# Performance work log

Measured on AMD Instinct MI355X. Metric: run time of the kernel, lower is better.

## Reference

```python
import jax, jax.numpy as jnp
import numpy as np

K = 100  # hard-coded in GWDLoss.forward


def _topk(scores, k=K):
    # CenterNet predict._topk: per-class topk then topk over classes.
    b, c, h, w = scores.shape
    topk_scores, topk_inds = jax.lax.top_k(scores.reshape(b, c, h * w), k)  # [b,c,k]
    topk_inds = topk_inds % (h * w)
    topk_ys = (topk_inds // w).astype(scores.dtype)
    topk_xs = (topk_inds % w).astype(scores.dtype)
    topk_score, topk_ind = jax.lax.top_k(topk_scores.reshape(b, c * k), k)  # [b,k]
    def g(t):
        return jnp.take_along_axis(t.reshape(b, c * k), topk_ind, axis=1)
    return topk_score, g(topk_inds), g(topk_xs), g(topk_ys)


def _transpose_and_gather_feat(feat, ind):
    b, c, h, w = feat.shape
    feat = feat.transpose(0, 2, 3, 1).reshape(b, h * w, c)  # [b,hw,c]
    idx = jnp.broadcast_to(ind[:, :, None], (b, ind.shape[1], c))
    return jnp.take_along_axis(feat, idx, axis=1)  # [b,K,c]


def xywhr2xyrs(xywhr):
    xywhr = xywhr.reshape(-1, 5)
    xy = xywhr[:, :2]
    wh = jnp.clip(xywhr[:, 2:4], 1e-7, 1e7)
    r = jnp.deg2rad(xywhr[:, 4])
    cos_r, sin_r = jnp.cos(r), jnp.sin(r)
    R = jnp.stack([cos_r, -sin_r, sin_r, cos_r], axis=-1).reshape(-1, 2, 2)
    S = 0.5 * wh[:, :, None] * jnp.eye(2, dtype=wh.dtype)  # diag_embed
    return xy, R, S


def gwd_loss(pred, target, tau=1.0, alpha=1.0):
    xy_p, R_p, S_p = xywhr2xyrs(pred)
    xy_t, R_t, S_t = xywhr2xyrs(target)
    xy_distance = jnp.sum((xy_p - xy_t) ** 2, axis=-1)
    Sigma_p = R_p @ (S_p ** 2) @ jnp.swapaxes(R_p, -1, -2)
    Sigma_t = R_t @ (S_t ** 2) @ jnp.swapaxes(R_t, -1, -2)
    dS_p = jnp.diagonal(S_p, axis1=-2, axis2=-1)
    dS_t = jnp.diagonal(S_t, axis1=-2, axis2=-1)
    whr = jnp.sum(dS_p ** 2, -1) + jnp.sum(dS_t ** 2, -1)
    _t = Sigma_p @ Sigma_t
    _t_tr = jnp.trace(_t, axis1=-2, axis2=-1)
    _t_det_sqrt = jnp.prod(dS_p, -1) * jnp.prod(dS_t, -1)
    whr = whr - 2.0 * jnp.sqrt(jnp.maximum(_t_tr + 2.0 * _t_det_sqrt, 0.0))
    distance = jnp.maximum(xy_distance + alpha * alpha * whr, 0.0)
    distance = jnp.log1p(distance)  # fun='log'
    return 1.0 - 1.0 / (tau + distance)  # tau=1.0 >= 1.0


def _forward(hm_p, ab_p, ang_p, hm_t, ab_t, ang_t, ind, reg_mask):
    mask = reg_mask.astype(jnp.float32)  # [B,K]
    pred_ab = _transpose_and_gather_feat(ab_p, ind)    # [B,K,2]
    pred_ang = _transpose_and_gather_feat(ang_p, ind)  # [B,K,1]
    mask_ab = mask[:, :, None]
    mask_ang = mask[:, :, None]
    _, _, xp, yp = _topk(hm_p)
    pred_xy = jnp.stack([xp, yp], axis=2)  # [B,K,2]
    pred = jnp.concatenate([pred_xy * mask_ab, pred_ab * 2.0 * mask_ab,
                            (pred_ang - 90.0) * mask_ang], axis=2)
    _, _, xt, yt = _topk(hm_t)
    target_xy = jnp.stack([xt, yt], axis=2)
    target = jnp.concatenate([target_xy * mask_ab, ab_t * 2.0 * mask_ab,
                              (ang_t - 90.0) * mask_ang], axis=2)
    return jnp.sum(gwd_loss(pred, target)) / (jnp.sum(mask) + 1e-8)


def setup_inputs() -> dict:
    key = jax.random.key(0)
    ks = jax.random.split(key, 8)
    B, H, W = 64, 256, 256
    return {
        "hm_p": jax.random.uniform(ks[0], (B, 1, H, W), jnp.float32),
        "ab_p": jax.random.uniform(ks[1], (B, 2, H, W), jnp.float32),
        "ang_p": jax.random.uniform(ks[2], (B, 1, H, W), jnp.float32),
        "hm_t": jax.random.uniform(ks[3], (B, 1, H, W), jnp.float32),
        "ab_t": jax.random.uniform(ks[4], (B, K, 2), jnp.float32),
        "ang_t": jax.random.uniform(ks[5], (B, K, 1), jnp.float32),
        "ind": jax.random.randint(ks[6], (B, K), 0, H * W, jnp.int32),
        "reg_mask": jax.random.randint(ks[7], (B, K), 0, 2, jnp.int32),
    }


def reference(hm_p, ab_p, ang_p, hm_t, ab_t, ang_t, ind, reg_mask):
    return _forward(hm_p, ab_p, ang_p, hm_t, ab_t, ang_t, ind, reg_mask)
```

## Files before the change

kernel.cpp:

```cpp
#include <hip/hip_runtime.h>
#include <stdint.h>

#define HW 65536
#define WIMG 256
#define TOPK 100
#define CAP2 2048
#define CAPC 256
#define NCHUNK 8
#define NGROUP 128
#define NPAIR 6400
#define FTHR 512

__device__ __forceinline__ uint32_t fkey(float v) {
    uint32_t b = __float_as_uint(v);
    return b ^ ((b & 0x80000000u) ? 0xFFFFFFFFu : 0x80000000u);
}

#define CAND_OFF  0
#define CNT_OFF   2097152
#define XY_OFF    2101248
#define PART_OFF  2203648
#define DONE_OFF  2204160
#define WS_FAST_BYTES 2204164

#define FILT_THR 0.9975f

#define AGENT __HIP_MEMORY_SCOPE_AGENT

__global__ __launch_bounds__(FTHR) void filter_kernel(
    const float* __restrict__ hm_p, const float* __restrict__ hm_t,
    unsigned long long* __restrict__ cand, uint32_t* __restrict__ chunkcnt)
{
    __shared__ unsigned long long lbuf[CAPC];
    __shared__ uint32_t lcnt;

    const int blk   = blockIdx.x;
    const int group = blk >> 3;
    const int chunk = blk & (NCHUNK - 1);
    const int which = group & 1;
    const int b     = group >> 1;
    const float* src = (which ? hm_t : hm_p) + (size_t)b * HW + chunk * (HW / NCHUNK);
    const float4* src4 = (const float4*)src;
    const int base0 = chunk * (HW / NCHUNK);

    if (threadIdx.x == 0) lcnt = 0;
    __syncthreads();

    #pragma unroll
    for (int t = 0; t < HW / NCHUNK / 4 / FTHR; ++t) {
        const int i = threadIdx.x + t * FTHR;
        float4 v = src4[i];
        const int base = base0 + i * 4;
        float f[4] = {v.x, v.y, v.z, v.w};
        #pragma unroll
        for (int e = 0; e < 4; ++e) {
            if (f[e] > FILT_THR) {
                uint32_t pos = atomicAdd(&lcnt, 1u);
                if (pos < CAPC)
                    lbuf[pos] = ((unsigned long long)fkey(f[e]) << 16) |
                                (unsigned long long)(65535 - (base + e));
            }
        }
    }
    __syncthreads();
    const uint32_t c = lcnt;
    if (threadIdx.x == 0) chunkcnt[blk] = c;
    unsigned long long* gc = cand + (size_t)blk * CAPC;
    for (uint32_t i = threadIdx.x; i < min(c, (uint32_t)CAPC); i += FTHR)
        gc[i] = lbuf[i];
}

__global__ __launch_bounds__(256) void sort_emit_kernel(
    const float* __restrict__ hm_p, const float* __restrict__ hm_t,
    const unsigned long long* __restrict__ cand, const uint32_t* __restrict__ chunkcnt,
    float* __restrict__ xy, uint32_t* __restrict__ done_cnt)
{
    __shared__ unsigned long long s[CAP2];
    __shared__ uint32_t s_cnt, s_kthr, s_klo, s_khi;

    const int tid   = threadIdx.x;
    const int group = blockIdx.x;
    const int which = group & 1;
    const int b     = group >> 1;

    if (group == 0 && tid == 0) *done_cnt = 0;

    uint32_t cs[NCHUNK];
    uint32_t total = 0;
    bool ok = true;
    #pragma unroll
    for (int k = 0; k < NCHUNK; ++k) {
        cs[k] = chunkcnt[group * NCHUNK + k];
        if (cs[k] > CAPC) ok = false;
        total += cs[k];
    }

    uint32_t c;
    if (ok && total >= TOPK && total <= CAP2) {
        uint32_t off = 0;
        #pragma unroll
        for (int k = 0; k < NCHUNK; ++k) {
            const unsigned long long* gc = cand + (size_t)(group * NCHUNK + k) * CAPC;
            for (uint32_t i = tid; i < cs[k]; i += 256) s[off + i] = gc[i];
            off += cs[k];
        }
        c = total;
    } else {
        const float* src = (which ? hm_t : hm_p) + (size_t)b * HW;
        const float4* src4 = (const float4*)src;
        if (tid == 0) { s_kthr = fkey(0.99f); s_klo = 0u; s_khi = 0xFFFFFFFFu; }
        __syncthreads();
        for (int it = 0; it < 48; ++it) {
            if (tid == 0) s_cnt = 0;
            __syncthreads();
            const uint32_t kthr = s_kthr;
            for (int t = 0; t < HW / 4 / 256; ++t) {
                float4 v = src4[tid + t * 256];
                const int base = (tid + t * 256) * 4;
                float f[4] = {v.x, v.y, v.z, v.w};
                #pragma unroll
                for (int e = 0; e < 4; ++e) {
                    uint32_t uk = fkey(f[e]);
                    if (uk > kthr) {
                        uint32_t pos = atomicAdd(&s_cnt, 1u);
                        if (pos < CAP2)
                            s[pos] = ((unsigned long long)uk << 16) |
                                     (unsigned long long)(65535 - (base + e));
                    }
                }
            }
            __syncthreads();
            const uint32_t cc = s_cnt;
            if (cc >= TOPK && cc <= CAP2) break;
            if (tid == 0) {
                if (cc < TOPK) { s_khi = s_kthr; s_kthr = s_klo + ((s_kthr - s_klo) >> 1); }
                else           { s_klo = s_kthr; s_kthr = s_kthr + ((s_khi - s_kthr) >> 1); }
            }
            __syncthreads();
        }
        c = min(s_cnt, (uint32_t)CAP2);
    }
    __syncthreads();

    int M = 128;
    while (M < (int)c) M <<= 1;
    for (int i = tid; i < M; i += 256) if (i >= (int)c) s[i] = 0ull;
    __syncthreads();

    for (int len = 2; len <= M; len <<= 1) {
        for (int inc = len >> 1; inc > 0; inc >>= 1) {
            for (int i = tid; i < M; i += 256) {
                int j = i ^ inc;
                if (j > i) {
                    bool desc = ((i & len) == 0);
                    unsigned long long a = s[i], d = s[j];
                    if ((a < d) == desc) { s[i] = d; s[j] = a; }
                }
            }
            __syncthreads();
        }
    }

    const int obase = which * 6400 + b * TOPK;
    for (int j = tid; j < TOPK; j += 256) {
        unsigned long long key = s[j];
        uint32_t idx = 65535u - (uint32_t)(key & 0xFFFFull);
        xy[obase + j]         = (float)(idx & (WIMG - 1));
        xy[12800 + obase + j] = (float)(idx >> 8);
    }
}

__device__ __forceinline__ float gwd(float px, float py, float pw, float ph, float pr,
                                     float tx, float ty, float tw, float th, float trg)
{
    pw = fminf(fmaxf(pw, 1e-7f), 1e7f);  ph = fminf(fmaxf(ph, 1e-7f), 1e7f);
    tw = fminf(fmaxf(tw, 1e-7f), 1e7f);  th = fminf(fmaxf(th, 1e-7f), 1e7f);
    const float d2r = 0.017453292519943295f;
    float rp = pr * d2r, rt = trg * d2r;
    float cp = cosf(rp), sp = sinf(rp);
    float ct = cosf(rt), st = sinf(rt);
    float ap = 0.5f * pw, bp = 0.5f * ph;
    float at = 0.5f * tw, bt = 0.5f * th;
    float ap2 = ap * ap, bp2 = bp * bp, at2 = at * at, bt2 = bt * bt;
    float p00 = ap2 * cp * cp + bp2 * sp * sp;
    float p11 = ap2 * sp * sp + bp2 * cp * cp;
    float p01 = (ap2 - bp2) * cp * sp;
    float t00 = at2 * ct * ct + bt2 * st * st;
    float t11 = at2 * st * st + bt2 * ct * ct;
    float t01 = (at2 - bt2) * ct * st;
    float dx = px - tx, dy = py - ty;
    float xyd = dx * dx + dy * dy;
    float whr = ap2 + bp2 + at2 + bt2;
    float trc = p00 * t00 + 2.f * p01 * t01 + p11 * t11;
    float dets = (ap * bp) * (at * bt);
    whr -= 2.f * sqrtf(fmaxf(trc + 2.f * dets, 0.f));
    float dist = fmaxf(xyd + whr, 0.f);
    float d = log1pf(dist);
    return 1.f - 1.f / (1.f + d);
}

__global__ __launch_bounds__(128) void loss_final_kernel(
    const float* __restrict__ ab_p,  const float* __restrict__ ang_p,
    const float* __restrict__ ab_t,  const float* __restrict__ ang_t,
    const int*   __restrict__ ind,   const int*   __restrict__ reg_mask,
    const float* __restrict__ xy,    float* __restrict__ partials,
    uint32_t* __restrict__ done_cnt, float* __restrict__ out)
{
    const int b = blockIdx.x;
    const int j = threadIdx.x;
    float loss = 0.f, msum = 0.f;
    if (j < TOPK) {
        const int i = b * TOPK + j;
        float m = (float)reg_mask[i];
        msum = m;
        int id = ind[i];
        float xp = xy[i];
        float xt = xy[6400 + i];
        float yp = xy[12800 + i];
        float yt = xy[19200 + i];
        float ab0 = ab_p[(size_t)(b * 2 + 0) * HW + id];
        float ab1 = ab_p[(size_t)(b * 2 + 1) * HW + id];
        float ang = ang_p[(size_t)b * HW + id];
        float px = xp * m, py = yp * m;
        float pw = 2.f * ab0 * m, ph = 2.f * ab1 * m;
        float pr = (ang - 90.f) * m;
        float tx = xt * m, ty = yt * m;
        float tw = 2.f * ab_t[b * 200 + j * 2 + 0] * m;
        float th = 2.f * ab_t[b * 200 + j * 2 + 1] * m;
        float trg = (ang_t[i] - 90.f) * m;
        loss = gwd(px, py, pw, ph, pr, tx, ty, tw, th, trg);
    }
    #pragma unroll
    for (int off = 32; off > 0; off >>= 1) {
        loss += __shfl_down(loss, off);
        msum += __shfl_down(msum, off);
    }
    __shared__ float sl[2], sm[2];
    __shared__ uint32_t s_old;
    if ((threadIdx.x & 63) == 0) { sl[threadIdx.x >> 6] = loss; sm[threadIdx.x >> 6] = msum; }
    __syncthreads();
    if (threadIdx.x == 0) {
        __hip_atomic_store(&partials[b * 2],     sl[0] + sl[1], __ATOMIC_RELEASE, AGENT);
        __hip_atomic_store(&partials[b * 2 + 1], sm[0] + sm[1], __ATOMIC_RELEASE, AGENT);
        s_old = __hip_atomic_fetch_add(done_cnt, 1u, __ATOMIC_ACQ_REL, AGENT);
    }
    __syncthreads();
    if (s_old == 63u && threadIdx.x < 64) {
        float L = __hip_atomic_load(&partials[2 * threadIdx.x],     __ATOMIC_ACQUIRE, AGENT);
        float M = __hip_atomic_load(&partials[2 * threadIdx.x + 1], __ATOMIC_ACQUIRE, AGENT);
        #pragma unroll
        for (int off = 32; off > 0; off >>= 1) {
            L += __shfl_down(L, off);
            M += __shfl_down(M, off);
        }
        if (threadIdx.x == 0) out[0] = L / (M + 1e-8f);
    }
}

#define XY_OFF2    0
#define PART_OFF2  102400
#define FDONE_OFF2 102912

__global__ __launch_bounds__(1024) void topk_sort_kernel(
    const float* __restrict__ hm_p, const float* __restrict__ hm_t,
    float* __restrict__ xy, uint32_t* __restrict__ fdone)
{
    __shared__ unsigned long long s[CAP2];
    __shared__ uint32_t lcnt, s_kthr, s_klo, s_khi;

    const int tid   = threadIdx.x;
    const int group = blockIdx.x;
    const int which = group & 1;
    const int b     = group >> 1;

    if (group == 0 && tid == 0) *fdone = 0u;

    const float* src = (which ? hm_t : hm_p) + (size_t)b * HW;
    const float4* src4 = (const float4*)src;

    if (tid == 0) lcnt = 0;
    __syncthreads();
    #pragma unroll 4
    for (int t = 0; t < HW / 4 / 1024; ++t) {
        const int i = tid + t * 1024;
        float4 v = src4[i];
        const int base = i * 4;
        float f[4] = {v.x, v.y, v.z, v.w};
        #pragma unroll
        for (int e = 0; e < 4; ++e) {
            if (f[e] > FILT_THR) {
                uint32_t pos = atomicAdd(&lcnt, 1u);
                if (pos < CAP2)
                    s[pos] = ((unsigned long long)fkey(f[e]) << 16) |
                             (unsigned long long)(65535 - (base + e));
            }
        }
    }
    __syncthreads();
    uint32_t c = lcnt;

    if (c < TOPK || c > CAP2) {
        if (tid == 0) { s_kthr = fkey(0.99f); s_klo = 0u; s_khi = 0xFFFFFFFFu; }
        __syncthreads();
        for (int it = 0; it < 48; ++it) {
            if (tid == 0) lcnt = 0;
            __syncthreads();
            const uint32_t kthr = s_kthr;
            for (int t = 0; t < HW / 4 / 1024; ++t) {
                float4 v = src4[tid + t * 1024];
                const int base = (tid + t * 1024) * 4;
                float f[4] = {v.x, v.y, v.z, v.w};
                #pragma unroll
                for (int e = 0; e < 4; ++e) {
                    uint32_t uk = fkey(f[e]);
                    if (uk > kthr) {
                        uint32_t pos = atomicAdd(&lcnt, 1u);
                        if (pos < CAP2)
                            s[pos] = ((unsigned long long)uk << 16) |
                                     (unsigned long long)(65535 - (base + e));
                    }
                }
            }
            __syncthreads();
            const uint32_t cc = lcnt;
            if (cc >= TOPK && cc <= CAP2) break;
            if (tid == 0) {
                if (cc < TOPK) { s_khi = s_kthr; s_kthr = s_klo + ((s_kthr - s_klo) >> 1); }
                else           { s_klo = s_kthr; s_kthr = s_kthr + ((s_khi - s_kthr) >> 1); }
            }
            __syncthreads();
        }
        c = min(lcnt, (uint32_t)CAP2);
        __syncthreads();
    }

    int M = 128;
    while (M < (int)c) M <<= 1;
    for (int i = tid; i < M; i += 1024) if (i >= (int)c) s[i] = 0ull;
    __syncthreads();
    for (int len = 2; len <= M; len <<= 1) {
        for (int inc = len >> 1; inc > 0; inc >>= 1) {
            for (int i = tid; i < M; i += 1024) {
                int j = i ^ inc;
                if (j > i) {
                    bool desc = ((i & len) == 0);
                    unsigned long long a = s[i], d = s[j];
                    if ((a < d) == desc) { s[i] = d; s[j] = a; }
                }
            }
            __syncthreads();
        }
    }
    const int obase = which * 6400 + b * TOPK;
    for (int j = tid; j < TOPK; j += 1024) {
        unsigned long long key = s[j];
        uint32_t idx = 65535u - (uint32_t)(key & 0xFFFFull);
        xy[obase + j]         = (float)(idx & (WIMG - 1));
        xy[12800 + obase + j] = (float)(idx >> 8);
    }
}

extern "C" void kernel_launch(void* const* d_in, const int* in_sizes, int n_in,
                              void* d_out, int out_size, void* d_ws, size_t ws_size,
                              hipStream_t stream)
{
    const float* hm_p  = (const float*)d_in[0];
    const float* ab_p  = (const float*)d_in[1];
    const float* ang_p = (const float*)d_in[2];
    const float* hm_t  = (const float*)d_in[3];
    const float* ab_t  = (const float*)d_in[4];
    const float* ang_t = (const float*)d_in[5];
    const int*   ind      = (const int*)d_in[6];
    const int*   reg_mask = (const int*)d_in[7];
    float* out = (float*)d_out;

    if (ws_size >= WS_FAST_BYTES) {
        unsigned long long* cand = (unsigned long long*)((char*)d_ws + CAND_OFF);
        uint32_t* cnt   = (uint32_t*)((char*)d_ws + CNT_OFF);
        float*    xy    = (float*)((char*)d_ws + XY_OFF);
        float*    part  = (float*)((char*)d_ws + PART_OFF);
        uint32_t* done  = (uint32_t*)((char*)d_ws + DONE_OFF);

        filter_kernel<<<NGROUP * NCHUNK, FTHR, 0, stream>>>(hm_p, hm_t, cand, cnt);
        sort_emit_kernel<<<NGROUP, 256, 0, stream>>>(hm_p, hm_t, cand, cnt, xy, done);
        loss_final_kernel<<<64, 128, 0, stream>>>(ab_p, ang_p, ab_t, ang_t, ind,
                                                  reg_mask, xy, part, done, out);
    } else {
        float*    xy    = (float*)((char*)d_ws + XY_OFF2);
        float*    part  = (float*)((char*)d_ws + PART_OFF2);
        uint32_t* fdone = (uint32_t*)((char*)d_ws + FDONE_OFF2);
        topk_sort_kernel<<<NGROUP, 1024, 0, stream>>>(hm_p, hm_t, xy, fdone);
        loss_final_kernel<<<64, 128, 0, stream>>>(ab_p, ang_p, ab_t, ang_t, ind,
                                                  reg_mask, xy, part, fdone, out);
    }
}
```

Before: 26.53 us.

## Replace bitonic sort with rank counting and shrink per-chunk candidate buffers

After: 21.43 us, median of 3. -19.2%, faster.

```diff
diff --git a/kernel.cpp b/kernel.cpp
--- a/kernel.cpp
+++ b/kernel.cpp
@@ -5,10 +5,9 @@
 #define WIMG 256
 #define TOPK 100
 #define CAP2 2048
-#define CAPC 256
+#define CAPC 64
 #define NCHUNK 8
 #define NGROUP 128
-#define NPAIR 6400
 #define FTHR 512
 
 __device__ __forceinline__ uint32_t fkey(float v) {
@@ -17,11 +16,11 @@
 }
 
 #define CAND_OFF  0
-#define CNT_OFF   2097152
-#define XY_OFF    2101248
-#define PART_OFF  2203648
-#define DONE_OFF  2204160
-#define WS_FAST_BYTES 2204164
+#define CNT_OFF   524288
+#define XY_OFF    528384
+#define PART_OFF  630784
+#define DONE_OFF  631296
+#define WS_FAST_BYTES 631300
 
 #define FILT_THR 0.9975f
 
@@ -66,8 +65,8 @@
     const uint32_t c = lcnt;
     if (threadIdx.x == 0) chunkcnt[blk] = c;
     unsigned long long* gc = cand + (size_t)blk * CAPC;
-    for (uint32_t i = threadIdx.x; i < min(c, (uint32_t)CAPC); i += FTHR)
-        gc[i] = lbuf[i];
+    if (threadIdx.x < min(c, (uint32_t)CAPC))
+        gc[threadIdx.x] = lbuf[threadIdx.x];
 }
 
 __global__ __launch_bounds__(256) void sort_emit_kernel(
@@ -76,6 +75,8 @@
     float* __restrict__ xy, uint32_t* __restrict__ done_cnt)
 {
     __shared__ unsigned long long s[CAP2];
+    __shared__ uint32_t s_cs[NCHUNK], s_off[NCHUNK];
+    __shared__ uint32_t s_meta[2];
     __shared__ uint32_t s_cnt, s_kthr, s_klo, s_khi;
 
     const int tid   = threadIdx.x;
@@ -85,26 +86,29 @@
 
     if (group == 0 && tid == 0) *done_cnt = 0;
 
-    uint32_t cs[NCHUNK];
-    uint32_t total = 0;
-    bool ok = true;
-    #pragma unroll
-    for (int k = 0; k < NCHUNK; ++k) {
-        cs[k] = chunkcnt[group * NCHUNK + k];
-        if (cs[k] > CAPC) ok = false;
-        total += cs[k];
-    }
-
-    uint32_t c;
-    if (ok && total >= TOPK && total <= CAP2) {
-        uint32_t off = 0;
+    if (tid < NCHUNK) s_cs[tid] = chunkcnt[group * NCHUNK + tid];
+    __syncthreads();
+    if (tid == 0) {
+        uint32_t off = 0; int ok = 1;
         #pragma unroll
         for (int k = 0; k < NCHUNK; ++k) {
-            const unsigned long long* gc = cand + (size_t)(group * NCHUNK + k) * CAPC;
-            for (uint32_t i = tid; i < cs[k]; i += 256) s[off + i] = gc[i];
-            off += cs[k];
-        }
-        c = total;
+            s_off[k] = off;
+            if (s_cs[k] > CAPC) ok = 0;
+            off += s_cs[k];
+        }
+        s_meta[0] = off;
+        s_meta[1] = (ok && off >= TOPK && off <= CAP2) ? 1u : 0u;
+    }
+    __syncthreads();
+
+    uint32_t c;
+    if (s_meta[1]) {
+        const int k  = tid >> 5;
+        const int i0 = tid & 31;
+        const unsigned long long* gc = cand + (size_t)(group * NCHUNK + k) * CAPC;
+        const uint32_t ck = s_cs[k], ofk = s_off[k];
+        for (uint32_t i = i0; i < ck; i += 32) s[ofk + i] = gc[i];
+        c = s_meta[0];
     } else {
         const float* src = (which ? hm_t : hm_p) + (size_t)b * HW;
         const float4* src4 = (const float4*)src;
@@ -142,31 +146,26 @@
     }
     __syncthreads();
 
-    int M = 128;
-    while (M < (int)c) M <<= 1;
-    for (int i = tid; i < M; i += 256) if (i >= (int)c) s[i] = 0ull;
-    __syncthreads();
-
-    for (int len = 2; len <= M; len <<= 1) {
-        for (int inc = len >> 1; inc > 0; inc >>= 1) {
-            for (int i = tid; i < M; i += 256) {
-                int j = i ^ inc;
-                if (j > i) {
-                    bool desc = ((i & len) == 0);
-                    unsigned long long a = s[i], d = s[j];
-                    if ((a < d) == desc) { s[i] = d; s[j] = a; }
-                }
-            }
-            __syncthreads();
-        }
-    }
-
     const int obase = which * 6400 + b * TOPK;
-    for (int j = tid; j < TOPK; j += 256) {
-        unsigned long long key = s[j];
-        uint32_t idx = 65535u - (uint32_t)(key & 0xFFFFull);
-        xy[obase + j]         = (float)(idx & (WIMG - 1));
-        xy[12800 + obase + j] = (float)(idx >> 8);
+
+    if (c < TOPK) {
+        for (int j = tid; j < TOPK; j += 256) {
+            xy[obase + j]         = 255.f;
+            xy[12800 + obase + j] = 255.f;
+        }
+        __syncthreads();
+    }
+
+    for (int i = tid; i < (int)c; i += 256) {
+        const unsigned long long mine = s[i];
+        int rank = 0;
+        for (int j = 0; j < (int)c; ++j)
+            rank += (s[j] > mine) ? 1 : 0;
+        if (rank < TOPK) {
+            uint32_t idx = 65535u - (uint32_t)(mine & 0xFFFFull);
+            xy[obase + rank]         = (float)(idx & (WIMG - 1));
+            xy[12800 + obase + rank] = (float)(idx >> 8);
+        }
     }
 }
 
```
